# Optimization experiments

Measured on AMD Instinct MI355X. Metric: run time of the kernel, lower is better.

The kernel has to match this reference:

```python
import jax, jax.numpy as jnp
import numpy as np

V, C, T_MAX, H, L = 32000, 256, 2048, 8, 4
HS = C // H          # head_size = 32
FFN = 256            # hard-coded in Encoder
CLS_H, N_OUT = 512, 10
B, T = 4, 2048
EPS = 1e-5


def _ln(x, g, b):
    mu = jnp.mean(x, axis=-1, keepdims=True)
    var = jnp.mean(jnp.square(x - mu), axis=-1, keepdims=True)
    return (x - mu) * jax.lax.rsqrt(var + EPS) * g + b


def setup_inputs() -> dict:
    key = jax.random.key(0)
    ks = jax.random.split(key, 16)
    s = 0.02
    return {
        "idx": jax.random.randint(ks[0], (B, T), 0, V),
        "tok_emb": jax.random.normal(ks[1], (V, C), jnp.float32) * s,
        "pos_emb": jax.random.normal(ks[2], (T_MAX, C), jnp.float32) * s,
        "Wq": jax.random.normal(ks[3], (L, H, C, HS), jnp.float32) * s,
        "Wk": jax.random.normal(ks[4], (L, H, C, HS), jnp.float32) * s,
        "Wv": jax.random.normal(ks[5], (L, H, C, HS), jnp.float32) * s,
        "Wproj": jax.random.normal(ks[6], (L, C, C), jnp.float32) * s,
        "bproj": jnp.zeros((L, C), jnp.float32),
        "ln1_g": jnp.ones((L, C), jnp.float32), "ln1_b": jnp.zeros((L, C), jnp.float32),
        "ln2_g": jnp.ones((L, C), jnp.float32), "ln2_b": jnp.zeros((L, C), jnp.float32),
        "W1": jax.random.normal(ks[7], (L, C, FFN), jnp.float32) * s,
        "b1": jnp.zeros((L, FFN), jnp.float32),
        "W2": jax.random.normal(ks[8], (L, FFN, C), jnp.float32) * s,
        "b2": jnp.zeros((L, C), jnp.float32),
        "lnf_g": jnp.ones((C,), jnp.float32), "lnf_b": jnp.zeros((C,), jnp.float32),
        "Wc1": jax.random.normal(ks[9], (C, CLS_H), jnp.float32) * s,
        "bc1": jnp.zeros((CLS_H,), jnp.float32),
        "Wc2": jax.random.normal(ks[10], (CLS_H, N_OUT), jnp.float32) * s,
        "bc2": jnp.zeros((N_OUT,), jnp.float32),
    }


def reference(idx, tok_emb, pos_emb, Wq, Wk, Wv, Wproj, bproj,
              ln1_g, ln1_b, ln2_g, ln2_b, W1, b1, W2, b2,
              lnf_g, lnf_b, Wc1, bc1, Wc2, bc2):
    Bc, Tc = idx.shape
    x = tok_emb[idx] + pos_emb[:Tc]                       # [B,T,C]
    scale = C ** (-0.5)                                   # NOTE: scales by n_embd, not head_size (faithful)
    for i in range(L):
        h = _ln(x, ln1_g[i], ln1_b[i])
        q = jnp.einsum('btc,hcd->bhtd', h, Wq[i])
        k = jnp.einsum('btc,hcd->bhtd', h, Wk[i])
        v = jnp.einsum('btc,hcd->bhtd', h, Wv[i])
        wei = jax.nn.softmax(jnp.einsum('bhtd,bhsd->bhts', q, k) * scale, axis=-1)
        o = jnp.einsum('bhts,bhsd->bhtd', wei, v)         # [B,H,T,HS]
        o = o.transpose(0, 2, 1, 3).reshape(Bc, Tc, C)    # concat heads
        x = x + jnp.einsum('btc,cd->btd', o, Wproj[i]) + bproj[i]
        h2 = _ln(x, ln2_g[i], ln2_b[i])
        f = jax.nn.relu(jnp.einsum('btc,cf->btf', h2, W1[i]) + b1[i])
        x = x + jnp.einsum('btf,fc->btc', f, W2[i]) + b2[i]
    x = _ln(x, lnf_g, lnf_b)
    emb = jnp.mean(x, axis=1)                             # [B,C] mean pool over T
    logits = jax.nn.relu(emb @ Wc1 + bc1) @ Wc2 + bc2
    return jax.nn.softmax(logits, axis=1)                 # [B, n_output]
```

## Files before the change

kernel.cpp:

```cpp
#include <hip/hip_runtime.h>
#include <hip/hip_bf16.h>

#define NTOK 8192
#define CDIM 256
#define TDIM 2048
#define BDIM 4
#define HDIM 8
#define HSZ  32
#define LNUM 4
#define BUF  (NTOK*CDIM)
#define QSTR 768
#define LC   0.0901684400056f

typedef __attribute__((ext_vector_type(8))) short short8v;
typedef __attribute__((ext_vector_type(4))) short short4v;
typedef __attribute__((ext_vector_type(4))) float float4v;

#if __has_builtin(__builtin_amdgcn_cvt_pk_bf16_f32)
static __device__ __forceinline__ unsigned pkbf(float a, float b){
  auto t = __builtin_amdgcn_cvt_pk_bf16_f32(a, b);
  union { decltype(t) v; unsigned u; } cv; cv.v = t;
  return cv.u;
}
static __device__ __forceinline__ short f2bs(float f){
  auto t = __builtin_amdgcn_cvt_pk_bf16_f32(f, f);
  union { decltype(t) v; unsigned u; } cv; cv.v = t;
  return (short)(cv.u & 0xFFFFu);
}
#else
static __device__ __forceinline__ short f2bs(float f){
  union { float f; unsigned u; } x; x.f = f;
  unsigned r = x.u + 0x7FFFu + ((x.u >> 16) & 1u);
  return (short)(r >> 16);
}
static __device__ __forceinline__ unsigned pkbf(float a, float b){
  union { float f; unsigned u; } x, y; x.f = a; y.f = b;
  unsigned ra = x.u + 0x7FFFu + ((x.u >> 16) & 1u);
  unsigned rb = y.u + 0x7FFFu + ((y.u >> 16) & 1u);
  return __builtin_amdgcn_perm(rb, ra, 0x07060302u);
}
#endif
#if __has_builtin(__builtin_amdgcn_exp2f)
static __device__ __forceinline__ float fexp2(float x){ return __builtin_amdgcn_exp2f(x); }
#else
static __device__ __forceinline__ float fexp2(float x){ return __expf(x*0.6931471805599453f); }
#endif

#if __has_builtin(__builtin_amdgcn_mfma_f32_16x16x16bf16_1k)
static __device__ __forceinline__ float4v mfma16(short4v a, short4v b, float4v c){
  return __builtin_amdgcn_mfma_f32_16x16x16bf16_1k(a, b, c, 0, 0, 0);
}
#else
static __device__ __forceinline__ float4v mfma16(short4v a, short4v b, float4v c){
  float4v d;
  asm volatile("v_mfma_f32_16x16x16_bf16 %0, %1, %2, %3\n\ts_nop 7\n\ts_nop 7"
               : "=v"(d) : "v"(a), "v"(b), "v"(c));
  return d;
}
#endif
static __device__ __forceinline__ float4v mfma32(short8v a, short8v b, float4v c){
  return __builtin_amdgcn_mfma_f32_16x16x32_bf16(a, b, c, 0, 0, 0);
}

static __device__ __forceinline__ int faddr(int n, int k){
  return ((n>>4)*8 + (k>>5))*512 + ((((k>>3)&3)<<4) + (n&15))*8 + (k&7);
}

__global__ __launch_bounds__(256) void k_prep_embed(
    const int* __restrict__ idx, const float* __restrict__ tok, const float* __restrict__ pos,
    const float* __restrict__ Wq, const float* __restrict__ Wk, const float* __restrict__ Wv,
    const float* __restrict__ Wp, const float* __restrict__ W1, const float* __restrict__ W2,
    const float* __restrict__ l1g, const float* __restrict__ l2g,
    const float* __restrict__ l1b, const float* __restrict__ l2b,
    const float* __restrict__ b1, const float* __restrict__ Wc1, const float* __restrict__ lnfg,
    const float* __restrict__ lnfb, const float* __restrict__ bc1,
    short* __restrict__ qkvT, short* __restrict__ wpT, short* __restrict__ w1T, short* __restrict__ w2T,
    float* __restrict__ bq, float* __restrict__ b1f, float* __restrict__ Wc1s, float* __restrict__ bc1f,
    float* __restrict__ x, short* __restrict__ y) {
  const int tid = threadIdx.x;
  const int id = blockIdx.x;
  if (id >= 513) {
    const int bid = id - 513;
    const int lane = tid & 63;
    const int bt = bid*4 + (tid >> 6);
    const int t = bt & (TDIM-1);
    float4 tv = *(const float4*)&tok[(size_t)idx[bt]*CDIM + lane*4];
    float4 pv = *(const float4*)&pos[(size_t)t*CDIM + lane*4];
    float4 v = make_float4(tv.x+pv.x, tv.y+pv.y, tv.z+pv.z, tv.w+pv.w);
    *(float4*)&x[(size_t)bt*CDIM + lane*4] = v;
    float s1 = (v.x+v.y) + (v.z+v.w);
    float s2 = fmaf(v.x,v.x, fmaf(v.y,v.y, fmaf(v.z,v.z, v.w*v.w)));
    #pragma unroll
    for (int off=32; off>0; off>>=1) { s1 += __shfl_xor(s1, off, 64); s2 += __shfl_xor(s2, off, 64); }
    float mean = s1*(1.f/CDIM);
    float inv  = rsqrtf(s2*(1.f/CDIM) - mean*mean + 1e-5f);
    float cc = -mean*inv;
    union { unsigned u[2]; short4v s; } o;
    o.u[0] = pkbf(fmaf(v.x,inv,cc), fmaf(v.y,inv,cc));
    o.u[1] = pkbf(fmaf(v.z,inv,cc), fmaf(v.w,inv,cc));
    *(short4v*)&y[(size_t)bt*CDIM + lane*4] = o.s;
    return;
  }
  if (id < 384) {
    __shared__ float tile[64][65];
    int l = id / 96, rr = id % 96;
    const float* src; short* dst; int n0, k0; bool qkvmode; int gsel; float nscale = 1.f;
    if (rr < 48) {
      int tn = rr >> 2, tk = rr & 3;
      n0 = tn*64; k0 = tk*64;
      const float* b3 = (n0 < 256) ? Wq : (n0 < 512 ? Wk : Wv);
      src = b3 + l*65536;
      dst = qkvT + (size_t)l*QSTR*256;
      qkvmode = true; gsel = 1;
      if (n0 < 256) nscale = LC;
    } else {
      int r2 = rr - 48;
      int mat = r2 >> 4, t = r2 & 15;
      int tn = t >> 2, tk = t & 3;
      n0 = tn*64; k0 = tk*64;
      const float* b3 = (mat == 0) ? Wp : (mat == 1 ? W1 : W2);
      src = b3 + l*65536;
      dst = (mat == 0 ? wpT : (mat == 1 ? w1T : w2T)) + l*65536;
      qkvmode = false; gsel = (mat == 1) ? 2 : 0;
    }
    const int cn = tid & 63, rk = tid >> 6;
    #pragma unroll
    for (int i = 0; i < 16; ++i) {
      int kk = rk + i*4;
      int n = n0 + cn, k = k0 + kk;
      float v;
      if (qkvmode) { int nn = n & 255; v = src[((nn>>5)*256 + k)*32 + (nn & 31)]; }
      else         { v = src[k*256 + n]; }
      if (gsel == 1)      v *= l1g[l*256 + k];
      else if (gsel == 2) v *= l2g[l*256 + k];
      tile[kk][cn] = v;
    }
    __syncthreads();
    #pragma unroll
    for (int i = 0; i < 16; ++i) {
      int nn = rk + i*4;
      dst[faddr(n0 + nn, k0 + cn)] = f2bs(tile[cn][nn] * nscale);
    }
  } else if (id < 448) {
    __shared__ float red[4][64];
    int bid = id - 384;
    int l = bid >> 4, seg = bid & 15;
    int o = seg*64 + (tid & 63), pp = tid >> 6;
    float s = 0.f;
    if (o < 768) {
      const float* W = (o < 256 ? Wq : (o < 512 ? Wk : Wv)) + l*65536;
      int nn = o & 255, h = nn >> 5, d = nn & 31;
      const float* bv = l1b + l*256;
      for (int k = pp*64; k < pp*64+64; ++k) s = fmaf(bv[k], W[(h*256 + k)*32 + d], s);
    } else {
      const float* W = W1 + l*65536;
      int n = o - 768;
      const float* bv = l2b + l*256;
      for (int k = pp*64; k < pp*64+64; ++k) s = fmaf(bv[k], W[k*256 + n], s);
    }
    red[pp][tid & 63] = s;
    __syncthreads();
    if (tid < 64) {
      float tot = red[0][tid]+red[1][tid]+red[2][tid]+red[3][tid];
      int oo = seg*64 + tid;
      if (oo < 768) bq[l*768 + oo] = tot * (oo < 256 ? LC : 1.f);
      else          b1f[l*256 + (oo-768)] = b1[l*256 + (oo-768)] + tot;
    }
  } else if (id < 512) {
    int base = (id-448)*2048;
    #pragma unroll
    for (int i=0;i<8;++i) {
      int idx2 = base + i*256 + tid;
      Wc1s[idx2] = Wc1[idx2] * lnfg[idx2 >> 9];
    }
  } else {
    for (int u = tid; u < 512; u += 256) {
      float s = bc1[u];
      for (int k=0;k<256;++k) s = fmaf(lnfb[k], Wc1[k*512+u], s);
      bc1f[u] = s;
    }
  }
}

template<int NF, bool BIAS, bool RELU, bool OUTBF16, bool ACCUM>
__global__ __launch_bounds__(64) void k_gemm3(const short* __restrict__ A,
    const short* __restrict__ Bt, const float* __restrict__ bias, void* __restrict__ Cv,
    int outstride) {
  const int lane = threadIdx.x;
  const int q4 = lane >> 4, r = lane & 15;
  const int blockRow = blockIdx.x * 32;
  const int blockCol = blockIdx.y * (NF*16);
  float4v acc[2][NF];
  #pragma unroll
  for (int i=0;i<2;++i)
    #pragma unroll
    for (int j=0;j<NF;++j) acc[i][j] = (float4v){0,0,0,0};
  #pragma unroll
  for (int k0 = 0; k0 < 256; k0 += 32) {
    short8v a0 = *(const short8v*)&A[(size_t)(blockRow +      r)*CDIM + k0 + q4*8];
    short8v a1 = *(const short8v*)&A[(size_t)(blockRow + 16 + r)*CDIM + k0 + q4*8];
    #pragma unroll
    for (int nf=0; nf<NF; ++nf) {
      short8v bf = *(const short8v*)&Bt[(size_t)(((blockCol>>4) + nf)*8 + (k0>>5))*512 + lane*8];
      acc[0][nf] = mfma32(a0, bf, acc[0][nf]);
      acc[1][nf] = mfma32(a1, bf, acc[1][nf]);
    }
  }
  #pragma unroll
  for (int mf=0; mf<2; ++mf)
    #pragma unroll
    for (int nf=0; nf<NF; ++nf) {
      int col = blockCol + nf*16 + r;
      float bb = BIAS ? bias[col] : 0.f;
      #pragma unroll
      for (int reg=0; reg<4; ++reg) {
        int row = blockRow + mf*16 + q4*4 + reg;
        float v = acc[mf][nf][reg] + bb;
        if (RELU) v = fmaxf(v, 0.f);
        size_t oi = (size_t)row*outstride + col;
        if (ACCUM)        ((float*)Cv)[oi] += v;
        else if (OUTBF16) ((short*)Cv)[oi] = f2bs(v);
        else              ((float*)Cv)[oi] = v;
      }
    }
}

template<bool LAST>
__global__ __launch_bounds__(1024, 4) void k_mlp(
    const short* __restrict__ A,
    const short* __restrict__ Bt,
    const float* __restrict__ bias,
    const short* __restrict__ W1t, const float* __restrict__ b1f,
    const short* __restrict__ W2t, const float* __restrict__ b2,
    float* __restrict__ X,
    const short* __restrict__ Wqkv,
    const float* __restrict__ bq,
    short* __restrict__ Qout) {
  __shared__ __align__(16) short Ys[32*264];
  __shared__ __align__(16) short Gs[32*264];
  __shared__ float S1[32][16], S2[32][16];
  const int tid = threadIdx.x;
  const int w = tid >> 6, lane = tid & 63;
  const int q4 = lane >> 4, r = lane & 15;
  const int row0 = blockIdx.x * 32;
  const int colw = w*16 + r;

  {
    short8v av = *(const short8v*)&A[(size_t)row0*CDIM + tid*8];
    *(short8v*)&Gs[(tid>>5)*264 + (tid&31)*8] = av;
  }
  __syncthreads();

  float4v acc0 = {0,0,0,0}, acc1 = {0,0,0,0};
  #pragma unroll
  for (int k=0;k<8;++k) {
    short8v b  = *(const short8v*)&Bt[(size_t)(w*8+k)*512 + lane*8];
    short8v a0 = *(const short8v*)&Gs[(     r)*264 + k*32 + q4*8];
    short8v a1 = *(const short8v*)&Gs[(16 + r)*264 + k*32 + q4*8];
    acc0 = mfma32(a0, b, acc0);
    acc1 = mfma32(a1, b, acc1);
  }
  float xv0[4], xv1[4];
  {
    float bb = bias[colw];
    #pragma unroll
    for (int reg=0; reg<4; ++reg) {
      float t0 = acc0[reg] + bb + X[(size_t)(row0 +      q4*4 + reg)*CDIM + colw];
      float t1 = acc1[reg] + bb + X[(size_t)(row0 + 16 + q4*4 + reg)*CDIM + colw];
      xv0[reg] = t0; xv1[reg] = t1;
      float s10 = t0, s20 = t0*t0, s11 = t1, s21 = t1*t1;
      #pragma unroll
      for (int off=1; off<16; off<<=1) {
        s10 += __shfl_xor(s10, off, 64); s20 += __shfl_xor(s20, off, 64);
        s11 += __shfl_xor(s11, off, 64); s21 += __shfl_xor(s21, off, 64);
      }
      if (r == 0) {
        S1[     q4*4 + reg][w] = s10; S2[     q4*4 + reg][w] = s20;
        S1[16 + q4*4 + reg][w] = s11; S2[16 + q4*4 + reg][w] = s21;
      }
    }
  }
  __syncthreads();
  #pragma unroll
  for (int reg=0; reg<4; ++reg) {
    int r0i = q4*4 + reg, r1i = 16 + q4*4 + reg;
    float s1=0.f, s2=0.f, t1=0.f, t2=0.f;
    #pragma unroll
    for (int j=0;j<16;++j) { s1 += S1[r0i][j]; s2 += S2[r0i][j]; t1 += S1[r1i][j]; t2 += S2[r1i][j]; }
    float mean = s1*(1.f/CDIM);
    float inv  = rsqrtf(s2*(1.f/CDIM) - mean*mean + 1e-5f);
    Ys[r0i*264 + colw] = f2bs(fmaf(xv0[reg], inv, -mean*inv));
    float mean2 = t1*(1.f/CDIM);
    float inv2  = rsqrtf(t2*(1.f/CDIM) - mean2*mean2 + 1e-5f);
    Ys[r1i*264 + colw] = f2bs(fmaf(xv1[reg], inv2, -mean2*inv2));
  }
  __syncthreads();

  acc0 = (float4v){0,0,0,0}; acc1 = (float4v){0,0,0,0};
  #pragma unroll
  for (int k=0;k<8;++k) {
    short8v b  = *(const short8v*)&W1t[(size_t)(w*8+k)*512 + lane*8];
    short8v a0 = *(const short8v*)&Ys[(     r)*264 + k*32 + q4*8];
    short8v a1 = *(const short8v*)&Ys[(16 + r)*264 + k*32 + q4*8];
    acc0 = mfma32(a0, b, acc0);
    acc1 = mfma32(a1, b, acc1);
  }
  {
    float g = b1f[colw];
    #pragma unroll
    for (int reg=0; reg<4; ++reg) {
      Gs[(     q4*4 + reg)*264 + colw] = f2bs(fmaxf(acc0[reg] + g, 0.f));
      Gs[(16 + q4*4 + reg)*264 + colw] = f2bs(fmaxf(acc1[reg] + g, 0.f));
    }
  }
  __syncthreads();

  acc0 = (float4v){0,0,0,0}; acc1 = (float4v){0,0,0,0};
  #pragma unroll
  for (int k=0;k<8;++k) {
    short8v b  = *(const short8v*)&W2t[(size_t)(w*8+k)*512 + lane*8];
    short8v a0 = *(const short8v*)&Gs[(     r)*264 + k*32 + q4*8];
    short8v a1 = *(const short8v*)&Gs[(16 + r)*264 + k*32 + q4*8];
    acc0 = mfma32(a0, b, acc0);
    acc1 = mfma32(a1, b, acc1);
  }
  {
    float bb2 = b2[colw];
    #pragma unroll
    for (int reg=0; reg<4; ++reg) {
      float t0 = acc0[reg] + bb2 + xv0[reg];
      float t1 = acc1[reg] + bb2 + xv1[reg];
      xv0[reg] = t0; xv1[reg] = t1;
      X[(size_t)(row0 +      q4*4 + reg)*CDIM + colw] = t0;
      X[(size_t)(row0 + 16 + q4*4 + reg)*CDIM + colw] = t1;
      if (!LAST) {
        float s10 = t0, s20 = t0*t0, s11 = t1, s21 = t1*t1;
        #pragma unroll
        for (int off=1; off<16; off<<=1) {
          s10 += __shfl_xor(s10, off, 64); s20 += __shfl_xor(s20, off, 64);
          s11 += __shfl_xor(s11, off, 64); s21 += __shfl_xor(s21, off, 64);
        }
        if (r == 0) {
          S1[     q4*4 + reg][w] = s10; S2[     q4*4 + reg][w] = s20;
          S1[16 + q4*4 + reg][w] = s11; S2[16 + q4*4 + reg][w] = s21;
        }
      }
    }
  }
  if (LAST) return;
  __syncthreads();
  #pragma unroll
  for (int reg=0; reg<4; ++reg) {
    int r0i = q4*4 + reg, r1i = 16 + q4*4 + reg;
    float s1=0.f, s2=0.f, t1=0.f, t2=0.f;
    #pragma unroll
    for (int j=0;j<16;++j) { s1 += S1[r0i][j]; s2 += S2[r0i][j]; t1 += S1[r1i][j]; t2 += S2[r1i][j]; }
    float mean = s1*(1.f/CDIM);
    float inv  = rsqrtf(s2*(1.f/CDIM) - mean*mean + 1e-5f);
    Ys[r0i*264 + colw] = f2bs(fmaf(xv0[reg], inv, -mean*inv));
    float mean2 = t1*(1.f/CDIM);
    float inv2  = rsqrtf(t2*(1.f/CDIM) - mean2*mean2 + 1e-5f);
    Ys[r1i*264 + colw] = f2bs(fmaf(xv1[reg], inv2, -mean2*inv2));
  }
  __syncthreads();

  {
    float4v qa0[3], qa1[3];
    #pragma unroll
    for (int j=0;j<3;++j) { qa0[j] = (float4v){0,0,0,0}; qa1[j] = (float4v){0,0,0,0}; }
    #pragma unroll
    for (int k=0;k<8;++k) {
      short8v ay0 = *(const short8v*)&Ys[(     r)*264 + k*32 + q4*8];
      short8v ay1 = *(const short8v*)&Ys[(16 + r)*264 + k*32 + q4*8];
      #pragma unroll
      for (int nf=0; nf<3; ++nf) {
        short8v b = *(const short8v*)&Wqkv[(size_t)((w*3+nf)*8 + k)*512 + lane*8];
        qa0[nf] = mfma32(ay0, b, qa0[nf]);
        qa1[nf] = mfma32(ay1, b, qa1[nf]);
      }
    }
    #pragma unroll
    for (int nf=0; nf<3; ++nf) {
      int col = (w*3+nf)*16 + r;
      float bb = bq[col];
      #pragma unroll
      for (int reg=0; reg<4; ++reg) {
        Qout[(size_t)(row0 +      q4*4 + reg)*QSTR + col] = f2bs(qa0[nf][reg] + bb);
        Qout[(size_t)(row0 + 16 + q4*4 + reg)*QSTR + col] = f2bs(qa1[nf][reg] + bb);
      }
    }
  }
}

#define KSS 40
#define VTS 140
__global__ __launch_bounds__(512) void k_attn6(const short* __restrict__ qkv,
    short* __restrict__ O) {
  __shared__ __align__(16) short Ks[2][128*KSS];
  __shared__ __align__(16) short Vt[2][32*VTS];
  const int tid = threadIdx.x;
  const int w = tid >> 6, lane = tid & 63;
  const int q4 = lane >> 4, r = lane & 15;
  const int b = blockIdx.z, h = blockIdx.y;
  const int rowbase = blockIdx.x*128 + w*16;
  short8v Qf = *(const short8v*)&qkv[((size_t)(b*TDIM + rowbase + r))*QSTR + h*HSZ + q4*8];
  float4v o0 = {0,0,0,0}, o1 = {0,0,0,0};
  float l0 = 0.f;
  const bool isV = tid >= 256;
  const int t2 = tid & 255;
  const int kkey = t2 >> 1, kd0 = (t2 & 1)*16;
  const int kp = t2 & 63, dg = t2 >> 6;
  const short* kvbase = qkv + (size_t)b*TDIM*QSTR + h*HSZ;
  short8v ka, kb2, va, vb;
  if (isV) {
    va = *(const short8v*)&kvbase[(size_t)(2*kp)*QSTR   + 2*CDIM + dg*8];
    vb = *(const short8v*)&kvbase[(size_t)(2*kp+1)*QSTR + 2*CDIM + dg*8];
  } else {
    ka  = *(const short8v*)&kvbase[(size_t)kkey*QSTR + CDIM + kd0];
    kb2 = *(const short8v*)&kvbase[(size_t)kkey*QSTR + CDIM + kd0 + 8];
  }
  int p = 0;
  for (int s0 = 0; s0 < TDIM; s0 += 128, p ^= 1) {
    if (isV) {
      union { short8v s; unsigned u[4]; } A, C;
      A.s = va; C.s = vb;
      #pragma unroll
      for (int j=0;j<4;++j) {
        *(unsigned*)&Vt[p][(dg*8+2*j  )*VTS + 2*kp] = __builtin_amdgcn_perm(C.u[j], A.u[j], 0x05040100u);
        *(unsigned*)&Vt[p][(dg*8+2*j+1)*VTS + 2*kp] = __builtin_amdgcn_perm(C.u[j], A.u[j], 0x07060302u);
      }
    } else {
      *(short8v*)&Ks[p][kkey*KSS + kd0]     = ka;
      *(short8v*)&Ks[p][kkey*KSS + kd0 + 8] = kb2;
    }
    if (s0 + 128 < TDIM) {
      const short* nb = kvbase + (size_t)(s0+128)*QSTR;
      if (isV) {
        va = *(const short8v*)&nb[(size_t)(2*kp)*QSTR   + 2*CDIM + dg*8];
        vb = *(const short8v*)&nb[(size_t)(2*kp+1)*QSTR + 2*CDIM + dg*8];
      } else {
        ka  = *(const short8v*)&nb[(size_t)kkey*QSTR + CDIM + kd0];
        kb2 = *(const short8v*)&nb[(size_t)kkey*QSTR + CDIM + kd0 + 8];
      }
    }
    __syncthreads();
    #pragma unroll
    for (int ks = 0; ks < 8; ++ks) {
      short8v Kf = *(const short8v*)&Ks[p][(ks*16 + r)*KSS + q4*8];
      float4v sv = mfma32(Kf, Qf, (float4v){0,0,0,0});
      short4v Vf0 = *(const short4v*)&Vt[p][r*VTS + ks*16 + q4*4];
      short4v Vf1 = *(const short4v*)&Vt[p][(16+r)*VTS + ks*16 + q4*4];
      float p0 = fexp2(sv[0]), p1 = fexp2(sv[1]);
      float p2 = fexp2(sv[2]), p3 = fexp2(sv[3]);
      l0 += (p0+p1) + (p2+p3);
      union { unsigned u[2]; short4v s; } P;
      P.u[0] = pkbf(p0, p1); P.u[1] = pkbf(p2, p3);
      o0 = mfma16(P.s, Vf0, o0);
      o1 = mfma16(P.s, Vf1, o1);
    }
  }
  l0 += __shfl_xor(l0, 16, 64); l0 += __shfl_xor(l0, 32, 64);
  #pragma unroll
  for (int reg=0; reg<4; ++reg) {
    int qrow = q4*4 + reg;
    float i0 = 1.f / __shfl(l0, qrow, 64);
    short* op = O + ((size_t)(b*TDIM + rowbase + qrow))*CDIM + h*HSZ;
    op[r]    = f2bs(o0[reg]*i0);
    op[16+r] = f2bs(o1[reg]*i0);
  }
}

__global__ __launch_bounds__(256) void k_poolln(const float* __restrict__ X, float* __restrict__ part) {
  __shared__ float red[4][256];
  int b = blockIdx.x >> 3, chunk = blockIdx.x & 7;
  int wv = threadIdx.x >> 6, lane = threadIdx.x & 63;
  int base = b*TDIM + chunk*256 + wv*64;
  float a0=0,a1=0,a2=0,a3=0;
  for (int rr=0; rr<64; ++rr) {
    float4 v = *(const float4*)&X[(size_t)(base+rr)*CDIM + lane*4];
    float s1 = (v.x+v.y)+(v.z+v.w);
    float s2 = fmaf(v.x,v.x, fmaf(v.y,v.y, fmaf(v.z,v.z, v.w*v.w)));
    #pragma unroll
    for (int off=32; off>0; off>>=1) { s1 += __shfl_xor(s1,off,64); s2 += __shfl_xor(s2,off,64); }
    float mean = s1*(1.f/256.f);
    float inv  = rsqrtf(s2*(1.f/256.f) - mean*mean + 1e-5f);
    a0 = fmaf(v.x-mean, inv, a0); a1 = fmaf(v.y-mean, inv, a1);
    a2 = fmaf(v.z-mean, inv, a2); a3 = fmaf(v.w-mean, inv, a3);
  }
  red[wv][lane*4+0]=a0; red[wv][lane*4+1]=a1; red[wv][lane*4+2]=a2; red[wv][lane*4+3]=a3;
  __syncthreads();
  int c = threadIdx.x;
  part[blockIdx.x*256 + c] = (red[0][c]+red[1][c]+red[2][c]+red[3][c]) * (1.f/2048.f);
}

__global__ __launch_bounds__(512) void k_cls(const float* __restrict__ part,
    const float* __restrict__ Wc1s, const float* __restrict__ bc1f,
    const float* __restrict__ Wc2, const float* __restrict__ bc2, float* __restrict__ out) {
  __shared__ float se[4][256];
  __shared__ float sh[4][512];
  __shared__ float red[160];
  __shared__ float sl[40];
  const int t = threadIdx.x;
  for (int j=t; j<1024; j+=512) {
    int b = j >> 8, c = j & 255;
    float s = 0.f;
    #pragma unroll
    for (int ch=0; ch<8; ++ch) s += part[(b*8+ch)*256 + c];
    se[b][c] = s;
  }
  __syncthreads();
  {
    float bb = bc1f[t];
    float a0=bb, a1=bb, a2=bb, a3=bb;
    for (int c=0; c<256; ++c) {
      float w2 = Wc1s[c*512 + t];
      a0 = fmaf(se[0][c], w2, a0); a1 = fmaf(se[1][c], w2, a1);
      a2 = fmaf(se[2][c], w2, a2); a3 = fmaf(se[3][c], w2, a3);
    }
    sh[0][t]=fmaxf(a0,0.f); sh[1][t]=fmaxf(a1,0.f);
    sh[2][t]=fmaxf(a2,0.f); sh[3][t]=fmaxf(a3,0.f);
  }
  __syncthreads();
  if (t < 160) {
    int o = t >> 2, pp = t & 3;
    int b = o / 10, j = o - b*10;
    const float* hp = &sh[b][pp*128];
    float s = 0.f;
    #pragma unroll 8
    for (int u=0; u<128; ++u) s = fmaf(hp[u], Wc2[(pp*128+u)*10 + j], s);
    red[t] = s;
  }
  __syncthreads();
  if (t < 40) sl[t] = (red[t*4]+red[t*4+1]) + (red[t*4+2]+red[t*4+3]) + bc2[t%10];
  __syncthreads();
  if (t < 4) {
    float mx = -1e30f;
    for (int j=0;j<10;++j) mx = fmaxf(mx, sl[t*10+j]);
    float e[10], sum = 0.f;
    for (int j=0;j<10;++j) { e[j] = __expf(sl[t*10+j]-mx); sum += e[j]; }
    float inv = 1.f/sum;
    for (int j=0;j<10;++j) out[t*10+j] = e[j]*inv;
  }
}

extern "C" void kernel_launch(void* const* d_in, const int* in_sizes, int n_in,
                              void* d_out, int out_size, void* d_ws, size_t ws_size,
                              hipStream_t stream) {
  const int*   idx = (const int*)d_in[0];
  const float* tok = (const float*)d_in[1];
  const float* pos = (const float*)d_in[2];
  const float* Wq  = (const float*)d_in[3];
  const float* Wk  = (const float*)d_in[4];
  const float* Wv  = (const float*)d_in[5];
  const float* Wp  = (const float*)d_in[6];
  const float* bp  = (const float*)d_in[7];
  const float* l1g = (const float*)d_in[8];
  const float* l1b = (const float*)d_in[9];
  const float* l2g = (const float*)d_in[10];
  const float* l2b = (const float*)d_in[11];
  const float* W1  = (const float*)d_in[12];
  const float* b1  = (const float*)d_in[13];
  const float* W2  = (const float*)d_in[14];
  const float* b2  = (const float*)d_in[15];
  const float* lfg = (const float*)d_in[16];
  const float* lfb = (const float*)d_in[17];
  const float* Wc1 = (const float*)d_in[18];
  const float* bc1 = (const float*)d_in[19];
  const float* Wc2 = (const float*)d_in[20];
  const float* bc2 = (const float*)d_in[21];

  char* p = (char*)d_ws;
  float* xb   = (float*)p;              p += (size_t)BUF*4;
  short* hb   = (short*)p;              p += (size_t)BUF*2;
  short* qkvb = (short*)p;              p += (size_t)NTOK*QSTR*2;
  float* part = (float*)p;              p += 32*256*4;
  short* wqkvT = (short*)p;             p += (size_t)LNUM*QSTR*256*2;
  short* wpT   = (short*)p;             p += (size_t)LNUM*65536*2;
  short* w1T   = (short*)p;             p += (size_t)LNUM*65536*2;
  short* w2T   = (short*)p;             p += (size_t)LNUM*65536*2;
  float* bq    = (float*)p;             p += (size_t)LNUM*768*4;
  float* b1f   = (float*)p;             p += (size_t)LNUM*256*4;
  float* Wc1s  = (float*)p;             p += (size_t)256*512*4;
  float* bc1f  = (float*)p;             p += 512*4;

  k_prep_embed<<<513 + NTOK/4, 256, 0, stream>>>(idx, tok, pos,
                                   Wq, Wk, Wv, Wp, W1, W2, l1g, l2g, l1b, l2b,
                                   b1, Wc1, lfg, lfb, bc1,
                                   wqkvT, wpT, w1T, w2T, bq, b1f, Wc1s, bc1f,
                                   xb, hb);
  k_gemm3<4,true,false,true,false><<<dim3(256,12), 64, 0, stream>>>(
      hb, wqkvT, bq, qkvb, QSTR);
  for (int l = 0; l < LNUM; ++l) {
    k_attn6<<<dim3(16, HDIM, BDIM), 512, 0, stream>>>(qkvb, hb);
    if (l < LNUM-1) {
      k_mlp<false><<<256, 1024, 0, stream>>>(
          hb, wpT + (size_t)l*65536, bp + l*CDIM,
          w1T + (size_t)l*65536, b1f + l*CDIM, w2T + (size_t)l*65536, b2 + l*CDIM,
          xb,
          wqkvT + (size_t)(l+1)*QSTR*256, bq + (l+1)*768, qkvb);
    } else {
      k_mlp<true><<<256, 1024, 0, stream>>>(
          hb, wpT + (size_t)l*65536, bp + l*CDIM,
          w1T + (size_t)l*65536, b1f + l*CDIM, w2T + (size_t)l*65536, b2 + l*CDIM,
          xb,
          wqkvT, bq, qkvb);
    }
  }
  k_poolln<<<32, 256, 0, stream>>>(xb, part);
  k_cls<<<1, 512, 0, stream>>>(part, Wc1s, bc1f, Wc2, bc2, (float*)d_out);
}
```

Baseline: 461.3 us.

## Shrink attention blocks to 256 threads and double grid, add trailing barrier

Attention blocks now cover 64 query rows with 256 threads instead of 128 rows with 512, and the grid doubles along the sequence axis. Each K/V staging thread loads twice as much data per tile. A second barrier at the end of each tile iteration guards the double-buffered shared memory against early overwrite. This aims for finer-grained scheduling and better occupancy, at the cost of more global K/V traffic and an extra synchronization per tile.

```diff
diff --git a/kernel.cpp b/kernel.cpp
--- a/kernel.cpp
+++ b/kernel.cpp
@@ -394,7 +394,7 @@
 
 #define KSS 40
 #define VTS 140
-__global__ __launch_bounds__(512) void k_attn6(const short* __restrict__ qkv,
+__global__ __launch_bounds__(256, 4) void k_attn6(const short* __restrict__ qkv,
     short* __restrict__ O) {
   __shared__ __align__(16) short Ks[2][128*KSS];
   __shared__ __align__(16) short Vt[2][32*VTS];
@@ -402,45 +402,61 @@
   const int w = tid >> 6, lane = tid & 63;
   const int q4 = lane >> 4, r = lane & 15;
   const int b = blockIdx.z, h = blockIdx.y;
-  const int rowbase = blockIdx.x*128 + w*16;
+  const int rowbase = blockIdx.x*64 + w*16;
   short8v Qf = *(const short8v*)&qkv[((size_t)(b*TDIM + rowbase + r))*QSTR + h*HSZ + q4*8];
   float4v o0 = {0,0,0,0}, o1 = {0,0,0,0};
   float l0 = 0.f;
-  const bool isV = tid >= 256;
-  const int t2 = tid & 255;
-  const int kkey = t2 >> 1, kd0 = (t2 & 1)*16;
-  const int kp = t2 & 63, dg = t2 >> 6;
+  const bool isV = tid >= 128;
+  const int t2 = tid & 127;
+  const int kp = t2 & 63, dgb = t2 >> 6;
   const short* kvbase = qkv + (size_t)b*TDIM*QSTR + h*HSZ;
-  short8v ka, kb2, va, vb;
+  short8v ka0, ka1, ka2, ka3;
+  short8v va0, vb0, va1, vb1;
   if (isV) {
-    va = *(const short8v*)&kvbase[(size_t)(2*kp)*QSTR   + 2*CDIM + dg*8];
-    vb = *(const short8v*)&kvbase[(size_t)(2*kp+1)*QSTR + 2*CDIM + dg*8];
+    va0 = *(const short8v*)&kvbase[(size_t)(2*kp)*QSTR   + 2*CDIM + dgb*8];
+    vb0 = *(const short8v*)&kvbase[(size_t)(2*kp+1)*QSTR + 2*CDIM + dgb*8];
+    va1 = *(const short8v*)&kvbase[(size_t)(2*kp)*QSTR   + 2*CDIM + (dgb+2)*8];
+    vb1 = *(const short8v*)&kvbase[(size_t)(2*kp+1)*QSTR + 2*CDIM + (dgb+2)*8];
   } else {
-    ka  = *(const short8v*)&kvbase[(size_t)kkey*QSTR + CDIM + kd0];
-    kb2 = *(const short8v*)&kvbase[(size_t)kkey*QSTR + CDIM + kd0 + 8];
+    ka0 = *(const short8v*)&kvbase[(size_t)t2*QSTR + CDIM +  0];
+    ka1 = *(const short8v*)&kvbase[(size_t)t2*QSTR + CDIM +  8];
+    ka2 = *(const short8v*)&kvbase[(size_t)t2*QSTR + CDIM + 16];
+    ka3 = *(const short8v*)&kvbase[(size_t)t2*QSTR + CDIM + 24];
   }
   int p = 0;
   for (int s0 = 0; s0 < TDIM; s0 += 128, p ^= 1) {
     if (isV) {
       union { short8v s; unsigned u[4]; } A, C;
-      A.s = va; C.s = vb;
+      A.s = va0; C.s = vb0;
       #pragma unroll
       for (int j=0;j<4;++j) {
-        *(unsigned*)&Vt[p][(dg*8+2*j  )*VTS + 2*kp] = __builtin_amdgcn_perm(C.u[j], A.u[j], 0x05040100u);
-        *(unsigned*)&Vt[p][(dg*8+2*j+1)*VTS + 2*kp] = __builtin_amdgcn_perm(C.u[j], A.u[j], 0x07060302u);
+        *(unsigned*)&Vt[p][(dgb*8+2*j  )*VTS + 2*kp] = __builtin_amdgcn_perm(C.u[j], A.u[j], 0x05040100u);
+        *(unsigned*)&Vt[p][(dgb*8+2*j+1)*VTS + 2*kp] = __builtin_amdgcn_perm(C.u[j], A.u[j], 0x07060302u);
+      }
+      A.s = va1; C.s = vb1;
+      #pragma unroll
+      for (int j=0;j<4;++j) {
+        *(unsigned*)&Vt[p][((dgb+2)*8+2*j  )*VTS + 2*kp] = __builtin_amdgcn_perm(C.u[j], A.u[j], 0x05040100u);
+        *(unsigned*)&Vt[p][((dgb+2)*8+2*j+1)*VTS + 2*kp] = __builtin_amdgcn_perm(C.u[j], A.u[j], 0x07060302u);
       }
     } else {
-      *(short8v*)&Ks[p][kkey*KSS + kd0]     = ka;
-      *(short8v*)&Ks[p][kkey*KSS + kd0 + 8] = kb2;
+      *(short8v*)&Ks[p][t2*KSS +  0] = ka0;
+      *(short8v*)&Ks[p][t2*KSS +  8] = ka1;
+      *(short8v*)&Ks[p][t2*KSS + 16] = ka2;
+      *(short8v*)&Ks[p][t2*KSS + 24] = ka3;
     }
     if (s0 + 128 < TDIM) {
       const short* nb = kvbase + (size_t)(s0+128)*QSTR;
       if (isV) {
-        va = *(const short8v*)&nb[(size_t)(2*kp)*QSTR   + 2*CDIM + dg*8];
-        vb = *(const short8v*)&nb[(size_t)(2*kp+1)*QSTR + 2*CDIM + dg*8];
+        va0 = *(const short8v*)&nb[(size_t)(2*kp)*QSTR   + 2*CDIM + dgb*8];
+        vb0 = *(const short8v*)&nb[(size_t)(2*kp+1)*QSTR + 2*CDIM + dgb*8];
+        va1 = *(const short8v*)&nb[(size_t)(2*kp)*QSTR   + 2*CDIM + (dgb+2)*8];
+        vb1 = *(const short8v*)&nb[(size_t)(2*kp+1)*QSTR + 2*CDIM + (dgb+2)*8];
       } else {
-        ka  = *(const short8v*)&nb[(size_t)kkey*QSTR + CDIM + kd0];
-        kb2 = *(const short8v*)&nb[(size_t)kkey*QSTR + CDIM + kd0 + 8];
+        ka0 = *(const short8v*)&nb[(size_t)t2*QSTR + CDIM +  0];
+        ka1 = *(const short8v*)&nb[(size_t)t2*QSTR + CDIM +  8];
+        ka2 = *(const short8v*)&nb[(size_t)t2*QSTR + CDIM + 16];
+        ka3 = *(const short8v*)&nb[(size_t)t2*QSTR + CDIM + 24];
       }
     }
     __syncthreads();
@@ -458,6 +474,7 @@
       o0 = mfma16(P.s, Vf0, o0);
       o1 = mfma16(P.s, Vf1, o1);
     }
+    __syncthreads();
   }
   l0 += __shfl_xor(l0, 16, 64); l0 += __shfl_xor(l0, 32, 64);
   #pragma unroll
@@ -591,7 +608,7 @@
   k_gemm3<4,true,false,true,false><<<dim3(256,12), 64, 0, stream>>>(
       hb, wqkvT, bq, qkvb, QSTR);
   for (int l = 0; l < LNUM; ++l) {
-    k_attn6<<<dim3(16, HDIM, BDIM), 512, 0, stream>>>(qkvb, hb);
+    k_attn6<<<dim3(32, HDIM, BDIM), 256, 0, stream>>>(qkvb, hb);
     if (l < LNUM-1) {
       k_mlp<false><<<256, 1024, 0, stream>>>(
           hb, wpT + (size_t)l*65536, bp + l*CDIM,
```

After: 509.1 us. 1.1x slower.

## Split attention over two KV halves and combine partials in separate kernel

Applied to the files above, without the earlier changes.

Attention blocks now each process half of the key/value sequence, doubling the grid so more blocks run across the CUs. Unnormalized fp32 partial outputs and row sums are written to workspace. A new combine kernel adds the halves, normalizes, and writes the bf16 output. This trades extra global traffic and a kernel launch per layer for more parallelism and a shorter serial loop per block.

```diff
diff --git a/kernel.cpp b/kernel.cpp
--- a/kernel.cpp
+++ b/kernel.cpp
@@ -395,13 +395,14 @@
 #define KSS 40
 #define VTS 140
 __global__ __launch_bounds__(512) void k_attn6(const short* __restrict__ qkv,
-    short* __restrict__ O) {
+    float* __restrict__ opart, float* __restrict__ lpart) {
   __shared__ __align__(16) short Ks[2][128*KSS];
   __shared__ __align__(16) short Vt[2][32*VTS];
   const int tid = threadIdx.x;
   const int w = tid >> 6, lane = tid & 63;
   const int q4 = lane >> 4, r = lane & 15;
-  const int b = blockIdx.z, h = blockIdx.y;
+  const int b = blockIdx.z & 3, half = blockIdx.z >> 2, h = blockIdx.y;
+  const int kv0 = half*1024;
   const int rowbase = blockIdx.x*128 + w*16;
   short8v Qf = *(const short8v*)&qkv[((size_t)(b*TDIM + rowbase + r))*QSTR + h*HSZ + q4*8];
   float4v o0 = {0,0,0,0}, o1 = {0,0,0,0};
@@ -413,14 +414,14 @@
   const short* kvbase = qkv + (size_t)b*TDIM*QSTR + h*HSZ;
   short8v ka, kb2, va, vb;
   if (isV) {
-    va = *(const short8v*)&kvbase[(size_t)(2*kp)*QSTR   + 2*CDIM + dg*8];
-    vb = *(const short8v*)&kvbase[(size_t)(2*kp+1)*QSTR + 2*CDIM + dg*8];
+    va = *(const short8v*)&kvbase[(size_t)(kv0 + 2*kp)*QSTR   + 2*CDIM + dg*8];
+    vb = *(const short8v*)&kvbase[(size_t)(kv0 + 2*kp+1)*QSTR + 2*CDIM + dg*8];
   } else {
-    ka  = *(const short8v*)&kvbase[(size_t)kkey*QSTR + CDIM + kd0];
-    kb2 = *(const short8v*)&kvbase[(size_t)kkey*QSTR + CDIM + kd0 + 8];
+    ka  = *(const short8v*)&kvbase[(size_t)(kv0 + kkey)*QSTR + CDIM + kd0];
+    kb2 = *(const short8v*)&kvbase[(size_t)(kv0 + kkey)*QSTR + CDIM + kd0 + 8];
   }
   int p = 0;
-  for (int s0 = 0; s0 < TDIM; s0 += 128, p ^= 1) {
+  for (int s0 = 0; s0 < 1024; s0 += 128, p ^= 1) {
     if (isV) {
       union { short8v s; unsigned u[4]; } A, C;
       A.s = va; C.s = vb;
@@ -433,8 +434,8 @@
       *(short8v*)&Ks[p][kkey*KSS + kd0]     = ka;
       *(short8v*)&Ks[p][kkey*KSS + kd0 + 8] = kb2;
     }
-    if (s0 + 128 < TDIM) {
-      const short* nb = kvbase + (size_t)(s0+128)*QSTR;
+    if (s0 + 128 < 1024) {
+      const short* nb = kvbase + (size_t)(kv0 + s0 + 128)*QSTR;
       if (isV) {
         va = *(const short8v*)&nb[(size_t)(2*kp)*QSTR   + 2*CDIM + dg*8];
         vb = *(const short8v*)&nb[(size_t)(2*kp+1)*QSTR + 2*CDIM + dg*8];
@@ -460,14 +461,31 @@
     }
   }
   l0 += __shfl_xor(l0, 16, 64); l0 += __shfl_xor(l0, 32, 64);
+  if (lane < 16)
+    lpart[(size_t)half*NTOK*HDIM + (size_t)(b*TDIM + rowbase + lane)*HDIM + h] = l0;
   #pragma unroll
   for (int reg=0; reg<4; ++reg) {
     int qrow = q4*4 + reg;
-    float i0 = 1.f / __shfl(l0, qrow, 64);
-    short* op = O + ((size_t)(b*TDIM + rowbase + qrow))*CDIM + h*HSZ;
-    op[r]    = f2bs(o0[reg]*i0);
-    op[16+r] = f2bs(o1[reg]*i0);
-  }
+    float* op = opart + (size_t)half*BUF + ((size_t)(b*TDIM + rowbase + qrow))*CDIM + h*HSZ;
+    op[r]    = o0[reg];
+    op[16+r] = o1[reg];
+  }
+}
+
+__global__ __launch_bounds__(256) void k_attncomb(const float* __restrict__ opart,
+    const float* __restrict__ lpart, short* __restrict__ O) {
+  int f = blockIdx.x*256 + threadIdx.x;
+  int bt = f >> 6;
+  int c4 = (f & 63)*4;
+  int h = c4 >> 5;
+  float l = lpart[(size_t)bt*HDIM + h] + lpart[(size_t)NTOK*HDIM + (size_t)bt*HDIM + h];
+  float inv = 1.f / l;
+  float4 a = *(const float4*)&opart[(size_t)bt*CDIM + c4];
+  float4 bv = *(const float4*)&opart[(size_t)BUF + (size_t)bt*CDIM + c4];
+  union { unsigned u[2]; short4v s; } o;
+  o.u[0] = pkbf((a.x+bv.x)*inv, (a.y+bv.y)*inv);
+  o.u[1] = pkbf((a.z+bv.z)*inv, (a.w+bv.w)*inv);
+  *(short4v*)&O[(size_t)bt*CDIM + c4] = o.s;
 }
 
 __global__ __launch_bounds__(256) void k_poolln(const float* __restrict__ X, float* __restrict__ part) {
@@ -582,6 +600,8 @@
   float* b1f   = (float*)p;             p += (size_t)LNUM*256*4;
   float* Wc1s  = (float*)p;             p += (size_t)256*512*4;
   float* bc1f  = (float*)p;             p += 512*4;
+  float* opart = (float*)p;             p += (size_t)2*BUF*4;
+  float* lpart = (float*)p;             p += (size_t)2*NTOK*HDIM*4;
 
   k_prep_embed<<<513 + NTOK/4, 256, 0, stream>>>(idx, tok, pos,
                                    Wq, Wk, Wv, Wp, W1, W2, l1g, l2g, l1b, l2b,
@@ -591,7 +611,8 @@
   k_gemm3<4,true,false,true,false><<<dim3(256,12), 64, 0, stream>>>(
       hb, wqkvT, bq, qkvb, QSTR);
   for (int l = 0; l < LNUM; ++l) {
-    k_attn6<<<dim3(16, HDIM, BDIM), 512, 0, stream>>>(qkvb, hb);
+    k_attn6<<<dim3(16, HDIM, BDIM*2), 512, 0, stream>>>(qkvb, opart, lpart);
+    k_attncomb<<<BUF/1024, 256, 0, stream>>>(opart, lpart, hb);
     if (l < LNUM-1) {
       k_mlp<false><<<256, 1024, 0, stream>>>(
           hb, wpT + (size_t)l*65536, bp + l*CDIM,
```

After: 473.7 us. +2.7%, slower.
